# Kernel tuning notes

Measured on AMD Instinct MI355X. Metric: run time of the kernel, lower is better.

## Reference

```python
import jax, jax.numpy as jnp
import numpy as np

F = 256   # nb_features
H = 8     # nb_heads
B = 4
S = 1024  # q_s == kv_s
SCALE = F ** 0.5  # module MULTIPLIES scores by sqrt(f) when scale=True


def setup_inputs() -> dict:
    key = jax.random.key(0)
    ks = jax.random.split(key, 6)
    return {
        "q_input": jax.random.normal(ks[0], (B, F, S), dtype=jnp.float32),
        "kv_input": jax.random.normal(ks[1], (B, F, S), dtype=jnp.float32),
        "Wq": jax.random.normal(ks[2], (F, F * H), dtype=jnp.float32) * (F ** -0.5),
        "Wk": jax.random.normal(ks[3], (F, F * H), dtype=jnp.float32) * (F ** -0.5),
        "Wv": jax.random.normal(ks[4], (F, F * H), dtype=jnp.float32) * (F ** -0.5),
        "Wz": jax.random.normal(ks[5], (F * H, F), dtype=jnp.float32) * ((F * H) ** -0.5),
    }


def reference(q_input, kv_input, Wq, Wk, Wv, Wz):
    b, f, q_s = q_input.shape
    kv_s = kv_input.shape[2]
    h = H
    # (b, f, s) -> (b, s, f)
    qx = jnp.transpose(q_input, (0, 2, 1))
    kvx = jnp.transpose(kv_input, (0, 2, 1))
    # Linear f -> f*h, then split last dim into (f, h)
    q = (qx @ Wq).reshape(b, q_s, f, h)
    k = (kvx @ Wk).reshape(b, kv_s, f, h)
    v = (kvx @ Wv).reshape(b, kv_s, f, h)
    # sigmoid-gated attention: scores MULTIPLIED by sqrt(f)
    qkt = jnp.einsum('bifh,bjfh->bijh', q, k)
    attn = jax.nn.sigmoid(qkt * SCALE)
    weighted_v = jnp.einsum('bijh,bjfh->bifh', attn, v)  # (b, q_s, f, h)
    z = weighted_v.reshape(b * q_s, f * h)
    out = jax.nn.relu(z @ Wz)  # dropout p=0.0 -> identity
    return jnp.transpose(out.reshape(b, q_s, f), (0, 2, 1))  # (b, f, q_s)
```

## Files before the change

### kernel.cpp

```cpp
#include <hip/hip_runtime.h>
#include <hip/hip_fp16.h>

typedef _Float16 f16;
typedef _Float16 f16x8 __attribute__((ext_vector_type(8)));
typedef float f32x4 __attribute__((ext_vector_type(4)));

#define AS1(p) ((const __attribute__((address_space(1))) void*)(p))
#define AS3(p) ((__attribute__((address_space(3))) void*)(p))

__device__ __forceinline__ void gload16(const void* g, void* l) {
  __builtin_amdgcn_global_load_lds(AS1(g), AS3(l), 16, 0, 0);
}

__device__ __forceinline__ float sgm(float x) {
  return __builtin_amdgcn_rcpf(1.0f + __builtin_amdgcn_exp2f(x * -23.083120654223414f));
}

__device__ __forceinline__ unsigned pack2(float a, float b) {
  union { f16 h[2]; unsigned u; } x;
  x.h[0] = (f16)a; x.h[1] = (f16)b;
  return x.u;
}

__device__ __forceinline__ void tbody(const float* __restrict__ ip,
                                      f16* __restrict__ op,
                                      long in_rs, long out_rs) {
  __shared__ float t[64][68];
  int tid = threadIdx.x;
  {
    int c4 = (tid & 15) * 4, r0 = tid >> 4;
#pragma unroll
    for (int p = 0; p < 4; ++p) {
      int r = r0 + 16 * p;
      float4 v = *(const float4*)(ip + (long)r * in_rs + c4);
      t[c4 + 0][r] = v.x; t[c4 + 1][r] = v.y; t[c4 + 2][r] = v.z; t[c4 + 3][r] = v.w;
    }
  }
  __syncthreads();
  {
    int r4 = (tid & 15) * 4, c0 = tid >> 4;
#pragma unroll
    for (int p = 0; p < 4; ++p) {
      int c = c0 + 16 * p;
      float4 v = *(const float4*)(&t[c][r4]);
      union { f16 h[4]; unsigned long long u; } pk;
      pk.h[0] = (f16)v.x; pk.h[1] = (f16)v.y; pk.h[2] = (f16)v.z; pk.h[3] = (f16)v.w;
      *(unsigned long long*)(op + (long)c * out_rs + r4) = pk.u;
    }
  }
}

__global__ __launch_bounds__(256) void tin(const float* __restrict__ qin,
                                           const float* __restrict__ kvin,
                                           f16* __restrict__ Xq, f16* __restrict__ Xkv) {
  int z = blockIdx.z;
  const float* in = (z < 4) ? qin : kvin;
  f16* out = (z < 4) ? Xq : Xkv;
  long b = z & 3;
  tbody(in + b * 262144 + (long)(blockIdx.y * 64) * 1024 + blockIdx.x * 64,
        out + b * 262144 + (long)(blockIdx.x * 64) * 256 + blockIdx.y * 64,
        1024, 256);
}

__global__ __launch_bounds__(256) void tw3(const float* __restrict__ Wq,
                                           const float* __restrict__ Wk,
                                           const float* __restrict__ Wv,
                                           f16* __restrict__ Wqt, f16* __restrict__ Wkt,
                                           f16* __restrict__ Wvt) {
  int z = blockIdx.z;
  const float* in = (z == 0) ? Wq : (z == 1) ? Wk : Wv;
  f16* out = (z == 0) ? Wqt : (z == 1) ? Wkt : Wvt;
  tbody(in + (long)(blockIdx.y * 64) * 2048 + blockIdx.x * 64,
        out + (long)(blockIdx.x * 64) * 256 + blockIdx.y * 64,
        2048, 256);
}

__global__ __launch_bounds__(256) void twz(const float* __restrict__ Wz,
                                           f16* __restrict__ Wzt) {
  long z = blockIdx.z;
  tbody(Wz + z * 256 + (long)(blockIdx.y * 64) * 2048 + blockIdx.x * 64,
        Wzt + z * 256 + (long)(blockIdx.x * 64) * 2048 + blockIdx.y * 64,
        2048, 2048);
}

__global__ __launch_bounds__(256) void projk(
    const f16* __restrict__ Xq, const f16* __restrict__ Xkv,
    const f16* __restrict__ Wqt, const f16* __restrict__ Wkt, const f16* __restrict__ Wvt,
    f16* __restrict__ Qh, f16* __restrict__ Kh, f16* __restrict__ Vt) {
  __shared__ char sm[65536];
  int z = blockIdx.z;
  const f16* A = (z == 0) ? Xq : Xkv;
  const f16* B = (z == 0) ? Wqt : (z == 1) ? Wkt : Wvt;
  int m0 = blockIdx.x * 128, n0 = blockIdx.y * 128;
  int tid = threadIdx.x, wave = tid >> 6, lane = tid & 63;
  int wm = wave & 1, wn = wave >> 1;
  f32x4 acc[4][4];
#pragma unroll
  for (int i = 0; i < 4; ++i)
#pragma unroll
    for (int j = 0; j < 4; ++j) acc[i][j] = (f32x4){0.f, 0.f, 0.f, 0.f};

  auto PSTAGE = [&](int buf, int kt) {
    char* As = sm + buf * 32768;
    char* Bs = As + 16384;
    int k0 = kt * 64;
#pragma unroll
    for (int is = 0; is < 4; ++is) {
      int loff = is * 4096 + wave * 1024;
      int g = loff + lane * 16;
      int row = g >> 7, sl = (g >> 4) & 7;
      int sp = (sl ^ (row & 7)) * 8;
      gload16(A + (long)(m0 + row) * 256 + k0 + sp, As + loff);
      gload16(B + (long)(n0 + row) * 256 + k0 + sp, Bs + loff);
    }
  };

  PSTAGE(0, 0);
  __syncthreads();
  for (int kt = 0; kt < 4; ++kt) {
    int cur = kt & 1;
    if (kt < 3) PSTAGE(cur ^ 1, kt + 1);
    const char* As = sm + cur * 32768;
    const char* Bs = As + 16384;
#pragma unroll
    for (int t = 0; t < 2; ++t) {
      f16x8 af[4], bf[4];
#pragma unroll
      for (int mi = 0; mi < 4; ++mi) {
        int row = wm * 64 + mi * 16 + (lane & 15);
        int sl = (t * 4 + (lane >> 4)) ^ (row & 7);
        af[mi] = *(const f16x8*)(As + row * 128 + sl * 16);
      }
#pragma unroll
      for (int ni = 0; ni < 4; ++ni) {
        int row = wn * 64 + ni * 16 + (lane & 15);
        int sl = (t * 4 + (lane >> 4)) ^ (row & 7);
        bf[ni] = *(const f16x8*)(Bs + row * 128 + sl * 16);
      }
#pragma unroll
      for (int mi = 0; mi < 4; ++mi)
#pragma unroll
        for (int ni = 0; ni < 4; ++ni)
          acc[mi][ni] = __builtin_amdgcn_mfma_f32_16x16x32_f16(af[mi], bf[ni], acc[mi][ni], 0, 0, 0);
    }
    __syncthreads();
  }
#pragma unroll
  for (int mi = 0; mi < 4; ++mi)
#pragma unroll
    for (int ni = 0; ni < 4; ++ni) {
      int cc = wn * 64 + ni * 16 + (lane & 15);
      int rs0 = wm * 64 + mi * 16 + (lane >> 4) * 4;
      union { f16 h[4]; unsigned long long u; } pk;
#pragma unroll
      for (int r = 0; r < 4; ++r) pk.h[r] = (f16)acc[mi][ni][r];
      *(unsigned long long*)(sm + cc * 272 + rs0 * 2) = pk.u;
    }
  __syncthreads();
  if (z < 2) {
    f16* outp = (z == 0) ? Qh : Kh;
#pragma unroll
    for (int pass = 0; pass < 4; ++pass) {
      int item = pass * 256 + tid;
      int rs = item & 127, h = item >> 7;
      int m = m0 + rs, b = m >> 10, s = m & 1023;
      union { unsigned short u16[16]; uint4 q[2]; } pk;
#pragma unroll
      for (int u = 0; u < 16; ++u)
        pk.u16[u] = *(const unsigned short*)(sm + (h + 8 * u) * 272 + rs * 2);
      f16* dst = outp + ((long)(b * 8 + h) * 1024 + s) * 256 + (n0 >> 3);
      *(uint4*)dst = pk.q[0];
      *(uint4*)(dst + 8) = pk.q[1];
    }
  } else {
    int cc = tid >> 1, half = tid & 1;
    int c = n0 + cc, h = c & 7, fi = c >> 3;
    int m = m0 + half * 64;
    int b = m >> 10, s0 = m & 1023;
    uint4 q[8];
#pragma unroll
    for (int j = 0; j < 8; ++j)
      q[j] = *(const uint4*)(sm + cc * 272 + half * 128 + j * 16);
    f16* dst = Vt + ((long)(b * 8 + h) * 256 + fi) * 1024 + s0;
#pragma unroll
    for (int j = 0; j < 8; ++j) *(uint4*)(dst + j * 8) = q[j];
  }
}

__global__ __launch_bounds__(256) void attnk(
    const f16* __restrict__ Qh, const f16* __restrict__ Kh,
    const f16* __restrict__ Vt, f16* __restrict__ Zb) {
  __shared__ char sm[65536];
  int flat = blockIdx.x;
  int xcd = flat & 7, slotb = flat >> 3;
  int bh = xcd + 8 * (slotb & 3);
  int i0 = (slotb >> 2) * 64;
  int tid = threadIdx.x, wave = tid >> 6, lane = tid & 63;
  int l15 = lane & 15, l4 = lane >> 4;
  const f16* Qp = Qh + (long)bh * 262144;
  const f16* Kp = Kh + (long)bh * 262144;
  const f16* Vp = Vt + (long)bh * 262144;
  f16x8 q[8];
  {
    const f16* qr = Qp + (long)(i0 + wave * 16 + l15) * 256 + l4 * 8;
#pragma unroll
    for (int t = 0; t < 8; ++t) q[t] = *(const f16x8*)(qr + t * 32);
  }
  f32x4 acc[16];
#pragma unroll
  for (int i = 0; i < 16; ++i) acc[i] = (f32x4){0.f, 0.f, 0.f, 0.f};

  auto STAGE = [&](int buf, int j0) {
    char* Ks = sm + buf * 32768;
    char* Vs = Ks + 16384;
#pragma unroll
    for (int is = 0; is < 4; ++is) {
      int loff = is * 4096 + wave * 1024;
      int g = loff + lane * 16;
      {
        int row = g >> 9, sl = (g >> 4) & 31;
        gload16(Kp + (long)(j0 + row) * 256 + ((sl ^ (row & 7)) * 8), Ks + loff);
      }
      {
        int row = g >> 6, sl = (g >> 4) & 3;
        gload16(Vp + (long)row * 1024 + j0 + ((sl ^ ((row >> 1) & 3)) * 8), Vs + loff);
      }
    }
  };

  STAGE(0, 0);
  __syncthreads();
  for (int jt = 0; jt < 32; ++jt) {
    int cur = jt & 1;
    if (jt < 31) STAGE(cur ^ 1, (jt + 1) * 32);
    const char* Ks = sm + cur * 32768;
    const char* Vs = Ks + 16384;
    f32x4 s0 = (f32x4){0.f, 0.f, 0.f, 0.f};
    f32x4 s1 = (f32x4){0.f, 0.f, 0.f, 0.f};
#pragma unroll
    for (int t = 0; t < 8; ++t) {
      int sl = (t * 4 + l4) ^ (l15 & 7);
      f16x8 k0 = *(const f16x8*)(Ks + l15 * 512 + sl * 16);
      f16x8 k1 = *(const f16x8*)(Ks + (16 + l15) * 512 + sl * 16);
      s0 = __builtin_amdgcn_mfma_f32_16x16x32_f16(k0, q[t], s0, 0, 0, 0);
      s1 = __builtin_amdgcn_mfma_f32_16x16x32_f16(k1, q[t], s1, 0, 0, 0);
    }
    unsigned u00 = pack2(sgm(s0[0]), sgm(s0[1]));
    unsigned u01 = pack2(sgm(s0[2]), sgm(s0[3]));
    unsigned u10 = pack2(sgm(s1[0]), sgm(s1[1]));
    unsigned u11 = pack2(sgm(s1[2]), sgm(s1[3]));
    auto a0 = __builtin_amdgcn_permlane32_swap(u00, u10, false, false);
    auto w02 = __builtin_amdgcn_permlane16_swap(a0[0], a0[1], false, false);
    auto a1 = __builtin_amdgcn_permlane32_swap(u01, u11, false, false);
    auto w13 = __builtin_amdgcn_permlane16_swap(a1[0], a1[1], false, false);
    union { unsigned u[4]; f16x8 v; } pa;
    pa.u[0] = w02[0]; pa.u[1] = w13[0]; pa.u[2] = w02[1]; pa.u[3] = w13[1];
#pragma unroll
    for (int nf = 0; nf < 16; ++nf) {
      int fr = nf * 16 + l15;
      int sl = l4 ^ ((fr >> 1) & 3);
      f16x8 vb = *(const f16x8*)(Vs + fr * 64 + sl * 16);
      acc[nf] = __builtin_amdgcn_mfma_f32_16x16x32_f16(pa.v, vb, acc[nf], 0, 0, 0);
    }
    __syncthreads();
  }
#pragma unroll
  for (int nf = 0; nf < 16; ++nf)
#pragma unroll
    for (int r = 0; r < 4; ++r) {
      int il = wave * 16 + l4 * 4 + r;
      int f = nf * 16 + l15;
      *(f16*)(sm + il * 512 + ((f * 2) ^ (((il >> 2) & 3) << 5))) = (f16)acc[nf][r];
    }
  __syncthreads();
  f16* zp = Zb + ((long)bh * 1024 + i0) * 256;
#pragma unroll
  for (int c = 0; c < 8; ++c) {
    int il = c * 8 + (tid >> 5);
    int fb = (tid & 31) * 16;
    uint4 v = *(const uint4*)(sm + il * 512 + (fb ^ (((il >> 2) & 3) << 5)));
    *(uint4*)((char*)zp + il * 512 + fb) = v;
  }
}

__global__ __launch_bounds__(256) void zkern(
    const f16* __restrict__ Wzt, const f16* __restrict__ Zb,
    float* __restrict__ out) {
  __shared__ char sm[32768];
  int fo0 = blockIdx.x * 64, s0 = blockIdx.y * 64, b = blockIdx.z;
  int tid = threadIdx.x, wave = tid >> 6, lane = tid & 63;
  int wm = wave & 1, wn = wave >> 1;
  f32x4 acc[2][2];
#pragma unroll
  for (int i = 0; i < 2; ++i)
#pragma unroll
    for (int j = 0; j < 2; ++j) acc[i][j] = (f32x4){0.f, 0.f, 0.f, 0.f};

  auto ZSTAGE = [&](int buf, int kt) {
    char* As = sm + buf * 16384;
    char* Bs = As + 8192;
    int k0 = kt * 64, h = k0 >> 8, fi0 = k0 & 255;
#pragma unroll
    for (int is = 0; is < 2; ++is) {
      int loff = is * 4096 + wave * 1024;
      int g = loff + lane * 16;
      int row = g >> 7, sl = (g >> 4) & 7;
      int sp = (sl ^ (row & 7)) * 8;
      gload16(Wzt + (long)(fo0 + row) * 2048 + k0 + sp, As + loff);
      gload16(Zb + ((long)(b * 8 + h) * 1024 + s0 + row) * 256 + fi0 + sp, Bs + loff);
    }
  };

  ZSTAGE(0, 0);
  __syncthreads();
  for (int kt = 0; kt < 32; ++kt) {
    int cur = kt & 1;
    if (kt < 31) ZSTAGE(cur ^ 1, kt + 1);
    const char* As = sm + cur * 16384;
    const char* Bs = As + 8192;
#pragma unroll
    for (int t = 0; t < 2; ++t) {
      f16x8 af[2], bf[2];
#pragma unroll
      for (int mi = 0; mi < 2; ++mi) {
        int row = wm * 32 + mi * 16 + (lane & 15);
        int sl = (t * 4 + (lane >> 4)) ^ (row & 7);
        af[mi] = *(const f16x8*)(As + row * 128 + sl * 16);
      }
#pragma unroll
      for (int ni = 0; ni < 2; ++ni) {
        int row = wn * 32 + ni * 16 + (lane & 15);
        int sl = (t * 4 + (lane >> 4)) ^ (row & 7);
        bf[ni] = *(const f16x8*)(Bs + row * 128 + sl * 16);
      }
#pragma unroll
      for (int mi = 0; mi < 2; ++mi)
#pragma unroll
        for (int ni = 0; ni < 2; ++ni)
          acc[mi][ni] = __builtin_amdgcn_mfma_f32_16x16x32_f16(af[mi], bf[ni], acc[mi][ni], 0, 0, 0);
    }
    __syncthreads();
  }
#pragma unroll
  for (int mi = 0; mi < 2; ++mi)
#pragma unroll
    for (int ni = 0; ni < 2; ++ni)
#pragma unroll
      for (int r = 0; r < 4; ++r) {
        int fo = fo0 + wm * 32 + mi * 16 + (lane >> 4) * 4 + r;
        int s = s0 + wn * 32 + ni * 16 + (lane & 15);
        float v = acc[mi][ni][r];
        out[((long)b * 256 + fo) * 1024 + s] = v > 0.f ? v : 0.f;
      }
}

extern "C" void kernel_launch(void* const* d_in, const int* in_sizes, int n_in,
                              void* d_out, int out_size, void* d_ws, size_t ws_size,
                              hipStream_t stream) {
  const float* qin = (const float*)d_in[0];
  const float* kvin = (const float*)d_in[1];
  const float* Wq = (const float*)d_in[2];
  const float* Wk = (const float*)d_in[3];
  const float* Wv = (const float*)d_in[4];
  const float* Wz = (const float*)d_in[5];
  float* out = (float*)d_out;
  char* ws = (char*)d_ws;
  const long MB = 1 << 20;
  f16* Xq  = (f16*)(ws + 0 * MB);
  f16* Xkv = (f16*)(ws + 2 * MB);
  f16* Wqt = (f16*)(ws + 4 * MB);
  f16* Wkt = (f16*)(ws + 5 * MB);
  f16* Wvt = (f16*)(ws + 6 * MB);
  f16* Wzt = (f16*)(ws + 7 * MB);
  f16* Qh  = (f16*)(ws + 8 * MB);
  f16* Kh  = (f16*)(ws + 24 * MB);
  f16* Vt  = (f16*)(ws + 40 * MB);
  f16* Zb  = Qh;
  dim3 blk(256);
  tin<<<dim3(16, 4, 8), blk, 0, stream>>>(qin, kvin, Xq, Xkv);
  tw3<<<dim3(32, 4, 3), blk, 0, stream>>>(Wq, Wk, Wv, Wqt, Wkt, Wvt);
  twz<<<dim3(4, 4, 8), blk, 0, stream>>>(Wz, Wzt);
  projk<<<dim3(32, 16, 3), blk, 0, stream>>>(Xq, Xkv, Wqt, Wkt, Wvt, Qh, Kh, Vt);
  attnk<<<dim3(512), blk, 0, stream>>>(Qh, Kh, Vt, Zb);
  zkern<<<dim3(4, 16, 4), blk, 0, stream>>>(Wzt, Zb, out);
}
```

Baseline: 126.3 us.

## Rewrite attention kernel with 32x32x16 MFMA and two waves per block

Restructures the attention kernel so each block runs two waves instead of four, with each wave covering 32 query rows using 32x32x16 MFMA tiles instead of 16x16x32. This raises arithmetic per LDS operand load and changes the K/V shared-memory layout and swizzle. The LDS-staged coalesced epilogue is dropped in favour of direct scattered f16 stores. The risks are fewer waves per block to hide latency, much higher register pressure from the larger accumulators, and uncoalesced 2-byte global writes.

Result: slower. 153.3 us (+21.4%).

```diff
diff --git a/kernel.cpp b/kernel.cpp
--- a/kernel.cpp
+++ b/kernel.cpp
@@ -4,6 +4,7 @@
 typedef _Float16 f16;
 typedef _Float16 f16x8 __attribute__((ext_vector_type(8)));
 typedef float f32x4 __attribute__((ext_vector_type(4)));
+typedef float f32x16 __attribute__((ext_vector_type(16)));
 
 #define AS1(p) ((const __attribute__((address_space(1))) void*)(p))
 #define AS3(p) ((__attribute__((address_space(3))) void*)(p))
@@ -187,43 +188,44 @@
   }
 }
 
-__global__ __launch_bounds__(256) void attnk(
+__global__ __launch_bounds__(128, 1) void attnk(
     const f16* __restrict__ Qh, const f16* __restrict__ Kh,
     const f16* __restrict__ Vt, f16* __restrict__ Zb) {
   __shared__ char sm[65536];
   int flat = blockIdx.x;
-  int xcd = flat & 7, slotb = flat >> 3;
-  int bh = xcd + 8 * (slotb & 3);
-  int i0 = (slotb >> 2) * 64;
+  int xcd = flat & 7, slot = flat >> 3;
+  int bh = xcd + 8 * (slot & 3);
+  int i0 = (slot >> 2) * 64;
   int tid = threadIdx.x, wave = tid >> 6, lane = tid & 63;
-  int l15 = lane & 15, l4 = lane >> 4;
+  int l31 = lane & 31, l5 = lane >> 5;
   const f16* Qp = Qh + (long)bh * 262144;
   const f16* Kp = Kh + (long)bh * 262144;
   const f16* Vp = Vt + (long)bh * 262144;
-  f16x8 q[8];
+  int iw = i0 + wave * 32;
+  f16x8 qf[16];
   {
-    const f16* qr = Qp + (long)(i0 + wave * 16 + l15) * 256 + l4 * 8;
-#pragma unroll
-    for (int t = 0; t < 8; ++t) q[t] = *(const f16x8*)(qr + t * 32);
-  }
-  f32x4 acc[16];
-#pragma unroll
-  for (int i = 0; i < 16; ++i) acc[i] = (f32x4){0.f, 0.f, 0.f, 0.f};
+    const f16* qr = Qp + (long)(iw + l31) * 256 + l5 * 8;
+#pragma unroll
+    for (int t = 0; t < 16; ++t) qf[t] = *(const f16x8*)(qr + t * 16);
+  }
+  f32x16 acc[8];
+#pragma unroll
+  for (int n = 0; n < 8; ++n)
+    acc[n] = (f32x16){0.f,0.f,0.f,0.f,0.f,0.f,0.f,0.f,0.f,0.f,0.f,0.f,0.f,0.f,0.f,0.f};
 
   auto STAGE = [&](int buf, int j0) {
     char* Ks = sm + buf * 32768;
     char* Vs = Ks + 16384;
 #pragma unroll
-    for (int is = 0; is < 4; ++is) {
-      int loff = is * 4096 + wave * 1024;
-      int g = loff + lane * 16;
+    for (int r = 0; r < 8; ++r) {
+      int o = r * 2048 + tid * 16;
       {
-        int row = g >> 9, sl = (g >> 4) & 31;
-        gload16(Kp + (long)(j0 + row) * 256 + ((sl ^ (row & 7)) * 8), Ks + loff);
+        int row = o >> 9, sl = (o >> 4) & 31;
+        gload16(Kp + (long)(j0 + row) * 256 + ((sl ^ row) * 8), Ks + o);
       }
       {
-        int row = g >> 6, sl = (g >> 4) & 3;
-        gload16(Vp + (long)row * 1024 + j0 + ((sl ^ ((row >> 1) & 3)) * 8), Vs + loff);
+        int jc = o >> 12, f = (o >> 4) & 255;
+        gload16(Vp + (long)f * 1024 + j0 + jc * 8, Vs + o);
       }
     }
   };
@@ -235,52 +237,41 @@
     if (jt < 31) STAGE(cur ^ 1, (jt + 1) * 32);
     const char* Ks = sm + cur * 32768;
     const char* Vs = Ks + 16384;
-    f32x4 s0 = (f32x4){0.f, 0.f, 0.f, 0.f};
-    f32x4 s1 = (f32x4){0.f, 0.f, 0.f, 0.f};
-#pragma unroll
-    for (int t = 0; t < 8; ++t) {
-      int sl = (t * 4 + l4) ^ (l15 & 7);
-      f16x8 k0 = *(const f16x8*)(Ks + l15 * 512 + sl * 16);
-      f16x8 k1 = *(const f16x8*)(Ks + (16 + l15) * 512 + sl * 16);
-      s0 = __builtin_amdgcn_mfma_f32_16x16x32_f16(k0, q[t], s0, 0, 0, 0);
-      s1 = __builtin_amdgcn_mfma_f32_16x16x32_f16(k1, q[t], s1, 0, 0, 0);
-    }
-    unsigned u00 = pack2(sgm(s0[0]), sgm(s0[1]));
-    unsigned u01 = pack2(sgm(s0[2]), sgm(s0[3]));
-    unsigned u10 = pack2(sgm(s1[0]), sgm(s1[1]));
-    unsigned u11 = pack2(sgm(s1[2]), sgm(s1[3]));
-    auto a0 = __builtin_amdgcn_permlane32_swap(u00, u10, false, false);
-    auto w02 = __builtin_amdgcn_permlane16_swap(a0[0], a0[1], false, false);
-    auto a1 = __builtin_amdgcn_permlane32_swap(u01, u11, false, false);
-    auto w13 = __builtin_amdgcn_permlane16_swap(a1[0], a1[1], false, false);
-    union { unsigned u[4]; f16x8 v; } pa;
-    pa.u[0] = w02[0]; pa.u[1] = w13[0]; pa.u[2] = w02[1]; pa.u[3] = w13[1];
-#pragma unroll
-    for (int nf = 0; nf < 16; ++nf) {
-      int fr = nf * 16 + l15;
-      int sl = l4 ^ ((fr >> 1) & 3);
-      f16x8 vb = *(const f16x8*)(Vs + fr * 64 + sl * 16);
-      acc[nf] = __builtin_amdgcn_mfma_f32_16x16x32_f16(pa.v, vb, acc[nf], 0, 0, 0);
+    f32x16 s = (f32x16){0.f,0.f,0.f,0.f,0.f,0.f,0.f,0.f,0.f,0.f,0.f,0.f,0.f,0.f,0.f,0.f};
+#pragma unroll
+    for (int t = 0; t < 16; ++t) {
+      int c = 2 * t + l5;
+      f16x8 kf = *(const f16x8*)(Ks + l31 * 512 + ((c ^ l31) * 16));
+      s = __builtin_amdgcn_mfma_f32_32x32x16_f16(kf, qf[t], s, 0, 0, 0);
+    }
+    unsigned u[8];
+#pragma unroll
+    for (int c2 = 0; c2 < 8; ++c2) u[c2] = pack2(sgm(s[2 * c2]), sgm(s[2 * c2 + 1]));
+    auto w0 = __builtin_amdgcn_permlane32_swap(u[0], u[2], false, false);
+    auto w1 = __builtin_amdgcn_permlane32_swap(u[1], u[3], false, false);
+    auto w2 = __builtin_amdgcn_permlane32_swap(u[4], u[6], false, false);
+    auto w3 = __builtin_amdgcn_permlane32_swap(u[5], u[7], false, false);
+    union { unsigned q[4]; f16x8 v; } A0, A1;
+    A0.q[0] = w0[0]; A0.q[1] = w1[0]; A0.q[2] = w0[1]; A0.q[3] = w1[1];
+    A1.q[0] = w2[0]; A1.q[1] = w3[0]; A1.q[2] = w2[1]; A1.q[3] = w3[1];
+#pragma unroll
+    for (int n = 0; n < 8; ++n) {
+      f16x8 v0 = *(const f16x8*)(Vs + (l5 * 256 + n * 32 + l31) * 16);
+      acc[n] = __builtin_amdgcn_mfma_f32_32x32x16_f16(A0.v, v0, acc[n], 0, 0, 0);
+      f16x8 v1 = *(const f16x8*)(Vs + ((2 + l5) * 256 + n * 32 + l31) * 16);
+      acc[n] = __builtin_amdgcn_mfma_f32_32x32x16_f16(A1.v, v1, acc[n], 0, 0, 0);
     }
     __syncthreads();
   }
-#pragma unroll
-  for (int nf = 0; nf < 16; ++nf)
-#pragma unroll
-    for (int r = 0; r < 4; ++r) {
-      int il = wave * 16 + l4 * 4 + r;
-      int f = nf * 16 + l15;
-      *(f16*)(sm + il * 512 + ((f * 2) ^ (((il >> 2) & 3) << 5))) = (f16)acc[nf][r];
-    }
-  __syncthreads();
-  f16* zp = Zb + ((long)bh * 1024 + i0) * 256;
-#pragma unroll
-  for (int c = 0; c < 8; ++c) {
-    int il = c * 8 + (tid >> 5);
-    int fb = (tid & 31) * 16;
-    uint4 v = *(const uint4*)(sm + il * 512 + (fb ^ (((il >> 2) & 3) << 5)));
-    *(uint4*)((char*)zp + il * 512 + fb) = v;
-  }
+  f16* zp = Zb + (long)bh * 262144;
+#pragma unroll
+  for (int n = 0; n < 8; ++n)
+#pragma unroll
+    for (int r = 0; r < 16; ++r) {
+      int i = iw + (r & 3) + 8 * (r >> 2) + 4 * l5;
+      int f = n * 32 + l31;
+      zp[(long)i * 256 + f] = (f16)acc[n][r];
+    }
 }
 
 __global__ __launch_bounds__(256) void zkern(
@@ -381,6 +372,6 @@
   tw3<<<dim3(32, 4, 3), blk, 0, stream>>>(Wq, Wk, Wv, Wqt, Wkt, Wvt);
   twz<<<dim3(4, 4, 8), blk, 0, stream>>>(Wz, Wzt);
   projk<<<dim3(32, 16, 3), blk, 0, stream>>>(Xq, Xkv, Wqt, Wkt, Wvt, Qh, Kh, Vt);
-  attnk<<<dim3(512), blk, 0, stream>>>(Qh, Kh, Vt, Zb);
+  attnk<<<dim3(512), dim3(128), 0, stream>>>(Qh, Kh, Vt, Zb);
   zkern<<<dim3(4, 16, 4), blk, 0, stream>>>(Wzt, Zb, out);
 }
```
